# Kernel tuning notes

Measured on AMD Instinct MI355X. Metric: run time of the kernel, lower is better.

Reference implementation:

```python
import jax, jax.numpy as jnp
import numpy as np

BN_EPS = 1e-5

def _bn_train(h, gamma, beta):
    # h: [B, V, P, C]; BatchNorm2d in training mode: stats over (B, V, P) per channel
    mean = jnp.mean(h, axis=(0, 1, 2), keepdims=True)
    var = jnp.var(h, axis=(0, 1, 2), keepdims=True)
    return (h - mean) * jax.lax.rsqrt(var + BN_EPS) * gamma + beta

def _vfe(h, keep, W, b, gamma, beta):
    # h: [B,V,P,Cin] -> [B,V,P,2*units]; keep: [B,V,P,1] (1 = valid point)
    h = jnp.einsum('bvpc,cu->bvpu', h, W) + b
    h = jax.nn.relu(_bn_train(h, gamma, beta))
    agg = jnp.max(h, axis=2, keepdims=True)                 # [B,V,1,units]
    out = jnp.concatenate([h, jnp.broadcast_to(agg, h.shape)], axis=-1)
    return out * keep

def setup_inputs() -> dict:
    key = jax.random.key(0)
    ks = jax.random.split(key, 16)
    B, V, P, C = 1, 20000, 35, 7
    D, H, W = 10, 200, 176
    x = jax.random.normal(ks[0], (B, V, P, C), dtype=jnp.float32)
    cz = jax.random.randint(ks[1], (B, V, 1), 0, D)
    cy = jax.random.randint(ks[2], (B, V, 1), 0, H)
    cx = jax.random.randint(ks[3], (B, V, 1), 0, W)
    coordinate = jnp.concatenate([cz, cy, cx], axis=-1).astype(jnp.int32)
    def kaiming(k, fan_in, shape):
        bound = np.sqrt(6.0 / fan_in)
        return jax.random.uniform(k, shape, jnp.float32, -bound, bound)
    return {
        'x': x, 'coordinate': coordinate,
        'W1': kaiming(ks[4], 7, (7, 16)), 'b1': jnp.zeros((16,), jnp.float32),
        'g1': jnp.ones((16,), jnp.float32), 'be1': jnp.zeros((16,), jnp.float32),
        'W2': kaiming(ks[5], 32, (32, 64)), 'b2': jnp.zeros((64,), jnp.float32),
        'g2': jnp.ones((64,), jnp.float32), 'be2': jnp.zeros((64,), jnp.float32),
        'Wd': kaiming(ks[6], 128, (128, 128)), 'bd': jnp.zeros((128,), jnp.float32),
        'gd': jnp.ones((128,), jnp.float32), 'bed': jnp.zeros((128,), jnp.float32),
    }

def reference(x, coordinate, W1, b1, g1, be1, W2, b2, g2, be2, Wd, bd, gd, bed):
    D, H, W = 10, 200, 176
    # mask == 1 where point is empty (all-zero features)
    empty = (jnp.sum(x, axis=-1) == 0.0)[..., None].astype(jnp.float32)
    keep = 1.0 - empty
    h = _vfe(x, keep, W1, b1, g1, be1)    # [B,V,P,32]
    h = _vfe(h, keep, W2, b2, g2, be2)    # [B,V,P,128]
    h = jnp.einsum('bvpc,cu->bvpu', h, Wd) + bd
    h = jax.nn.relu(_bn_train(h, gd, bed))
    h = jnp.max(h, axis=2)                # [B,V,128] (max over points)
    feats = jnp.transpose(h, (0, 2, 1))   # [B,128,V]
    def scatter_one(coords, f):
        # f: [128,V]; coords: [V,3]; scatter-add into [128,D,H,W]
        g = jnp.zeros((128, D, H, W), dtype=f.dtype)
        return g.at[:, coords[:, 0], coords[:, 1], coords[:, 2]].add(f)
    grid = jax.vmap(scatter_one)(coordinate, feats)  # [B,128,D,H,W]
    return grid
```

## Files before the change

### kernel.cpp

```cpp
#include <hip/hip_runtime.h>
#include <float.h>

#define NV   20000
#define NP   35
#define NPTS 700000

#define S1SUM 0
#define S1SQ  16
#define S2SUM 32
#define S2SQ  96
#define S3SUM 160
#define S3SQ  288
#define SC1   416
#define SH1   432
#define SC2   448
#define SH2   512
#define SC3   576
#define SH3   704
#define M3MAX 1024
#define M3MIN (1024 + NV*128)

__global__ __launch_bounds__(256) void k_stats1(const float* __restrict__ x,
    const float* __restrict__ W1, const float* __restrict__ b1, float* __restrict__ ws)
{
  __shared__ float sW1[112], sb1[16];
  __shared__ float red[4][32];
  int t = threadIdx.x;
  if (t < 112) sW1[t] = W1[t];
  if (t < 16)  sb1[t] = b1[t];
  __syncthreads();
  float s[16], ss[16];
  #pragma unroll
  for (int u=0;u<16;++u){ s[u]=0.f; ss[u]=0.f; }
  int stride = gridDim.x * blockDim.x;
  for (int p = blockIdx.x*blockDim.x + t; p < NPTS; p += stride) {
    float xv[7];
    #pragma unroll
    for (int c=0;c<7;++c) xv[c] = x[p*7+c];
    #pragma unroll
    for (int u=0;u<16;++u) {
      float h = sb1[u];
      #pragma unroll
      for (int c=0;c<7;++c) h = fmaf(xv[c], sW1[c*16+u], h);
      s[u] += h; ss[u] = fmaf(h,h,ss[u]);
    }
  }
  #pragma unroll
  for (int u=0;u<16;++u) {
    #pragma unroll
    for (int off=32; off>0; off>>=1) {
      s[u]  += __shfl_xor(s[u],  off);
      ss[u] += __shfl_xor(ss[u], off);
    }
  }
  int wid = t>>6, lane = t&63;
  if (lane == 0) {
    #pragma unroll
    for (int u=0;u<16;++u){ red[wid][u]=s[u]; red[wid][16+u]=ss[u]; }
  }
  __syncthreads();
  if (t < 32) {
    float a = red[0][t]+red[1][t]+red[2][t]+red[3][t];
    atomicAdd(&ws[S1SUM + t], a);
  }
}

__global__ void k_finalize(const float* __restrict__ sum, const float* __restrict__ sq,
    const float* __restrict__ g, const float* __restrict__ be,
    float* __restrict__ scale, float* __restrict__ shift, int C)
{
  int u = threadIdx.x;
  if (u < C) {
    const float invN = 1.f/(float)NPTS;
    float mean = sum[u]*invN;
    float var  = sq[u]*invN - mean*mean;
    float sc = g[u] * rsqrtf(var + 1e-5f);
    scale[u] = sc;
    shift[u] = fmaf(-mean, sc, be[u]);
  }
}

template<int STAGE>
__global__ __launch_bounds__(256) void k_pass(
    const float* __restrict__ x,
    const float* __restrict__ W1, const float* __restrict__ b1,
    const float* __restrict__ W2, const float* __restrict__ b2,
    const float* __restrict__ Wd, const float* __restrict__ bd,
    float* __restrict__ ws)
{
  constexpr int NW = 4;
  __shared__ float sW1[112], sb1v[16], ssc1[16], ssh1[16];
  __shared__ __align__(16) float h1n_lds[NW][NP][20];
  __shared__ float keep_lds[NW][NP + 1];
  __shared__ __align__(16) float h2n_lds[STAGE==3 ? NW : 1][STAGE==3 ? NP : 1][64];
  __shared__ __align__(16) float agg2_lds[STAGE==3 ? NW : 1][64];
  __shared__ __align__(16) float sWd[STAGE==3 ? 128*128 : 4];

  int t = threadIdx.x;
  if (t < 112) sW1[t] = W1[t];
  if (t < 16) { sb1v[t]=b1[t]; ssc1[t]=ws[SC1+t]; ssh1[t]=ws[SH1+t]; }
  if constexpr (STAGE==3) {
    for (int i = t*4; i < 128*128; i += 256*4)
      *reinterpret_cast<float4*>(&sWd[i]) = *reinterpret_cast<const float4*>(&Wd[i]);
  }
  __syncthreads();

  int lane = t & 63, w = t >> 6;
  float W2r[32];
  #pragma unroll
  for (int c=0;c<32;++c) W2r[c] = W2[c*64 + lane];
  float b2r = b2[lane];
  float sc2r=0.f, sh2r=0.f, bdr0=0.f, bdr1=0.f;
  if constexpr (STAGE==3) {
    sc2r = ws[SC2+lane]; sh2r = ws[SH2+lane];
    bdr0 = bd[lane]; bdr1 = bd[64+lane];
  }
  float s2=0.f, ss2=0.f;
  float s3a=0.f, ss3a=0.f, s3b=0.f, ss3b=0.f;
  float* m3x = ws + M3MAX;
  float* m3n = ws + M3MIN;

  int wave = (blockIdx.x * blockDim.x + t) >> 6;
  int nw = (gridDim.x * blockDim.x) >> 6;
  for (int v = wave; v < NV; v += nw) {
    int p = lane;
    float xv[7];
    float kp = 0.f;
    if (p < NP) {
      float sum = 0.f;
      #pragma unroll
      for (int c=0;c<7;++c){ xv[c] = x[(v*NP + p)*7 + c]; sum += xv[c]; }
      kp = (sum == 0.f) ? 0.f : 1.f;
    } else {
      #pragma unroll
      for (int c=0;c<7;++c) xv[c]=0.f;
    }
    float h1v[16];
    #pragma unroll
    for (int u=0;u<16;++u) h1v[u] = sb1v[u];
    #pragma unroll
    for (int c=0;c<7;++c){
      float xc = xv[c];
      #pragma unroll
      for (int u=0;u<16;++u) h1v[u] = fmaf(xc, sW1[c*16+u], h1v[u]);
    }
    float aggv[16];
    #pragma unroll
    for (int u=0;u<16;++u){
      float hn = fmaxf(0.f, fmaf(h1v[u], ssc1[u], ssh1[u]));
      h1v[u] = hn;
      aggv[u] = (p < NP) ? hn : -FLT_MAX;
    }
    #pragma unroll
    for (int u=0;u<16;++u){
      #pragma unroll
      for (int off=32; off>0; off>>=1)
        aggv[u] = fmaxf(aggv[u], __shfl_xor(aggv[u], off));
    }
    if (p < NP) {
      #pragma unroll
      for (int c=0;c<16;c+=4)
        *reinterpret_cast<float4*>(&h1n_lds[w][p][c]) =
            make_float4(h1v[c],h1v[c+1],h1v[c+2],h1v[c+3]);
      keep_lds[w][p] = kp;
    }
    float t1 = 0.f;
    #pragma unroll
    for (int c=0;c<16;++c) t1 = fmaf(aggv[c], W2r[16+c], t1);
    float agg2u = -FLT_MAX;
    #pragma unroll
    for (int p2=0;p2<NP;++p2){
      float kpp = keep_lds[w][p2];
      float d = t1;
      #pragma unroll
      for (int c=0;c<16;c+=4){
        float4 a = *reinterpret_cast<const float4*>(&h1n_lds[w][p2][c]);
        d = fmaf(a.x, W2r[c],   d);
        d = fmaf(a.y, W2r[c+1], d);
        d = fmaf(a.z, W2r[c+2], d);
        d = fmaf(a.w, W2r[c+3], d);
      }
      float h2p = fmaf(kpp, d, b2r);
      if constexpr (STAGE==2) {
        s2 += h2p; ss2 = fmaf(h2p, h2p, ss2);
      } else {
        float h2nv = fmaxf(0.f, fmaf(h2p, sc2r, sh2r));
        agg2u = fmaxf(agg2u, h2nv);
        h2n_lds[w][p2][lane] = h2nv;
      }
    }
    if constexpr (STAGE==3) {
      agg2_lds[w][lane] = agg2u;
      float t3a=0.f, t3b=0.f;
      #pragma unroll
      for (int c=0;c<64;++c){
        float a = agg2_lds[w][c];
        t3a = fmaf(a, sWd[(64+c)*128 + lane],      t3a);
        t3b = fmaf(a, sWd[(64+c)*128 + 64 + lane], t3b);
      }
      float acc0[NP], acc1[NP];
      #pragma unroll
      for (int p2=0;p2<NP;++p2){ acc0[p2]=0.f; acc1[p2]=0.f; }
      for (int cb=0; cb<64; cb+=4){
        float w00=sWd[(cb+0)*128+lane],    w01=sWd[(cb+1)*128+lane],
              w02=sWd[(cb+2)*128+lane],    w03=sWd[(cb+3)*128+lane];
        float w10=sWd[(cb+0)*128+64+lane], w11=sWd[(cb+1)*128+64+lane],
              w12=sWd[(cb+2)*128+64+lane], w13=sWd[(cb+3)*128+64+lane];
        #pragma unroll
        for (int p2=0;p2<NP;++p2){
          float4 a = *reinterpret_cast<const float4*>(&h2n_lds[w][p2][cb]);
          acc0[p2] = fmaf(a.x,w00, fmaf(a.y,w01, fmaf(a.z,w02, fmaf(a.w,w03, acc0[p2]))));
          acc1[p2] = fmaf(a.x,w10, fmaf(a.y,w11, fmaf(a.z,w12, fmaf(a.w,w13, acc1[p2]))));
        }
      }
      float mx0=-FLT_MAX, mx1=-FLT_MAX, mn0=FLT_MAX, mn1=FLT_MAX;
      #pragma unroll
      for (int p2=0;p2<NP;++p2){
        float kpp = keep_lds[w][p2];
        float h0 = fmaf(kpp, acc0[p2]+t3a, bdr0);
        float h1 = fmaf(kpp, acc1[p2]+t3b, bdr1);
        s3a += h0; ss3a = fmaf(h0,h0,ss3a);
        s3b += h1; ss3b = fmaf(h1,h1,ss3b);
        mx0=fmaxf(mx0,h0); mn0=fminf(mn0,h0);
        mx1=fmaxf(mx1,h1); mn1=fminf(mn1,h1);
      }
      m3x[v*128+lane]    = mx0;  m3x[v*128+64+lane] = mx1;
      m3n[v*128+lane]    = mn0;  m3n[v*128+64+lane] = mn1;
    }
  }
  if constexpr (STAGE==2) {
    atomicAdd(&ws[S2SUM+lane], s2);
    atomicAdd(&ws[S2SQ +lane], ss2);
  } else {
    atomicAdd(&ws[S3SUM+lane],    s3a);
    atomicAdd(&ws[S3SUM+64+lane], s3b);
    atomicAdd(&ws[S3SQ+lane],     ss3a);
    atomicAdd(&ws[S3SQ+64+lane],  ss3b);
  }
}

__global__ __launch_bounds__(256) void k_scatter(const float* __restrict__ ws,
    const int* __restrict__ coord, float* __restrict__ out)
{
  int tid = blockIdx.x*blockDim.x + threadIdx.x;
  if (tid >= NV*128) return;
  int v = tid >> 7, u = tid & 127;
  float sc = ws[SC3+u], sh = ws[SH3+u];
  float m = (sc >= 0.f) ? ws[M3MAX+tid] : ws[M3MIN+tid];
  float val = fmaxf(0.f, fmaf(m, sc, sh));
  if (val != 0.f) {
    int z = coord[v*3+0], y = coord[v*3+1], xx = coord[v*3+2];
    atomicAdd(&out[((u*10+z)*200+y)*176+xx], val);
  }
}

extern "C" void kernel_launch(void* const* d_in, const int* in_sizes, int n_in,
                              void* d_out, int out_size, void* d_ws, size_t ws_size,
                              hipStream_t stream)
{
  const float* x   = (const float*)d_in[0];
  const int*   coord = (const int*)d_in[1];
  const float* W1  = (const float*)d_in[2];
  const float* b1  = (const float*)d_in[3];
  const float* g1  = (const float*)d_in[4];
  const float* be1 = (const float*)d_in[5];
  const float* W2  = (const float*)d_in[6];
  const float* b2  = (const float*)d_in[7];
  const float* g2  = (const float*)d_in[8];
  const float* be2 = (const float*)d_in[9];
  const float* Wd  = (const float*)d_in[10];
  const float* bd  = (const float*)d_in[11];
  const float* gd  = (const float*)d_in[12];
  const float* bed = (const float*)d_in[13];
  float* out = (float*)d_out;
  float* ws  = (float*)d_ws;

  hipMemsetAsync(ws, 0, 416*sizeof(float), stream);
  hipMemsetAsync(out, 0, (size_t)out_size*sizeof(float), stream);

  k_stats1<<<640,256,0,stream>>>(x, W1, b1, ws);
  k_finalize<<<1,128,0,stream>>>(ws+S1SUM, ws+S1SQ, g1, be1, ws+SC1, ws+SH1, 16);
  k_pass<2><<<1024,256,0,stream>>>(x, W1,b1,W2,b2,Wd,bd, ws);
  k_finalize<<<1,128,0,stream>>>(ws+S2SUM, ws+S2SQ, g2, be2, ws+SC2, ws+SH2, 64);
  k_pass<3><<<512,256,0,stream>>>(x, W1,b1,W2,b2,Wd,bd, ws);
  k_finalize<<<1,128,0,stream>>>(ws+S3SUM, ws+S3SQ, gd, bed, ws+SC3, ws+SH3, 128);
  k_scatter<<<(NV*128+255)/256,256,0,stream>>>(ws, coord, out);
}
```

Measured before the change: 986.8 us.

## Compute layer-1 BN stats from input moments and fold finalize kernels into consumers

Replaces the layer-1 stats kernel with one that accumulates the first and second moments of the 7 input channels (35 values). Each consumer block then derives the layer-1 mean and variance analytically from W1. The three tiny finalize launches are removed and their scale/shift computation is done redundantly at the start of the consuming kernels. Stage 3 moves to 512-thread blocks (8 waves) with half the grid, and the h1 LDS padding is shrunk from 20 to 16. This cuts launches and per-point matmul work in the stats pass, but E[x^2]-based variance may lose float precision, and the larger stage-3 blocks change occupancy and LDS use.

```diff
diff --git a/kernel.cpp b/kernel.cpp
--- a/kernel.cpp
+++ b/kernel.cpp
@@ -5,102 +5,103 @@
 #define NP   35
 #define NPTS 700000
 
-#define S1SUM 0
-#define S1SQ  16
 #define S2SUM 32
 #define S2SQ  96
 #define S3SUM 160
 #define S3SQ  288
-#define SC1   416
-#define SH1   432
-#define SC2   448
-#define SH2   512
-#define SC3   576
-#define SH3   704
+#define MOM   864
 #define M3MAX 1024
 #define M3MIN (1024 + NV*128)
 
-__global__ __launch_bounds__(256) void k_stats1(const float* __restrict__ x,
-    const float* __restrict__ W1, const float* __restrict__ b1, float* __restrict__ ws)
-{
-  __shared__ float sW1[112], sb1[16];
-  __shared__ float red[4][32];
+__global__ __launch_bounds__(256) void k_moments(const float* __restrict__ x,
+                                                 float* __restrict__ ws)
+{
+  float m[35];
+  #pragma unroll
+  for (int i=0;i<35;++i) m[i]=0.f;
+  int stride = gridDim.x*blockDim.x;
+  for (int p = blockIdx.x*blockDim.x + threadIdx.x; p < NPTS; p += stride) {
+    float xv[7];
+    #pragma unroll
+    for (int c=0;c<7;++c) xv[c]=x[p*7+c];
+    #pragma unroll
+    for (int c=0;c<7;++c) m[c] += xv[c];
+    int k=7;
+    #pragma unroll
+    for (int c=0;c<7;++c)
+      #pragma unroll
+      for (int d=c; d<7; ++d){ m[k]=fmaf(xv[c],xv[d],m[k]); ++k; }
+  }
+  #pragma unroll
+  for (int i=0;i<35;++i){
+    #pragma unroll
+    for (int off=32;off>0;off>>=1) m[i]+=__shfl_xor(m[i],off);
+  }
+  __shared__ float red[4][35];
+  int t=threadIdx.x, wv=t>>6, ln=t&63;
+  if (ln==0){
+    #pragma unroll
+    for (int i=0;i<35;++i) red[wv][i]=m[i];
+  }
+  __syncthreads();
+  if (t<35) atomicAdd(&ws[MOM+t], red[0][t]+red[1][t]+red[2][t]+red[3][t]);
+}
+
+template<int STAGE>
+__global__ __launch_bounds__(STAGE==3?512:256) void k_pass(
+    const float* __restrict__ x,
+    const float* __restrict__ W1, const float* __restrict__ b1,
+    const float* __restrict__ g1, const float* __restrict__ be1,
+    const float* __restrict__ W2, const float* __restrict__ b2,
+    const float* __restrict__ g2, const float* __restrict__ be2,
+    const float* __restrict__ Wd, const float* __restrict__ bd,
+    float* __restrict__ ws)
+{
+  constexpr int NW = (STAGE==3) ? 8 : 4;
+  constexpr int NT = NW*64;
+  __shared__ float sW1[112], sb1v[16], ssc1[16], ssh1[16];
+  __shared__ float ssc2[STAGE==3?64:1], ssh2[STAGE==3?64:1];
+  __shared__ __align__(16) float h1n_lds[NW][NP][16];
+  __shared__ float keep_lds[NW][NP+1];
+  __shared__ __align__(16) float h2n_lds[STAGE==3?NW:1][STAGE==3?NP:1][64];
+  __shared__ float agg2_lds[STAGE==3?NW:1][64];
+  __shared__ __align__(16) float sWd[STAGE==3?128*128:4];
+
   int t = threadIdx.x;
   if (t < 112) sW1[t] = W1[t];
-  if (t < 16)  sb1[t] = b1[t];
-  __syncthreads();
-  float s[16], ss[16];
-  #pragma unroll
-  for (int u=0;u<16;++u){ s[u]=0.f; ss[u]=0.f; }
-  int stride = gridDim.x * blockDim.x;
-  for (int p = blockIdx.x*blockDim.x + t; p < NPTS; p += stride) {
-    float xv[7];
-    #pragma unroll
-    for (int c=0;c<7;++c) xv[c] = x[p*7+c];
-    #pragma unroll
-    for (int u=0;u<16;++u) {
-      float h = sb1[u];
-      #pragma unroll
-      for (int c=0;c<7;++c) h = fmaf(xv[c], sW1[c*16+u], h);
-      s[u] += h; ss[u] = fmaf(h,h,ss[u]);
-    }
-  }
-  #pragma unroll
-  for (int u=0;u<16;++u) {
-    #pragma unroll
-    for (int off=32; off>0; off>>=1) {
-      s[u]  += __shfl_xor(s[u],  off);
-      ss[u] += __shfl_xor(ss[u], off);
-    }
-  }
-  int wid = t>>6, lane = t&63;
-  if (lane == 0) {
-    #pragma unroll
-    for (int u=0;u<16;++u){ red[wid][u]=s[u]; red[wid][16+u]=ss[u]; }
-  }
-  __syncthreads();
-  if (t < 32) {
-    float a = red[0][t]+red[1][t]+red[2][t]+red[3][t];
-    atomicAdd(&ws[S1SUM + t], a);
-  }
-}
-
-__global__ void k_finalize(const float* __restrict__ sum, const float* __restrict__ sq,
-    const float* __restrict__ g, const float* __restrict__ be,
-    float* __restrict__ scale, float* __restrict__ shift, int C)
-{
-  int u = threadIdx.x;
-  if (u < C) {
+  if (t < 16) {
+    sb1v[t] = b1[t];
     const float invN = 1.f/(float)NPTS;
-    float mean = sum[u]*invN;
-    float var  = sq[u]*invN - mean*mean;
-    float sc = g[u] * rsqrtf(var + 1e-5f);
-    scale[u] = sc;
-    shift[u] = fmaf(-mean, sc, be[u]);
-  }
-}
-
-template<int STAGE>
-__global__ __launch_bounds__(256) void k_pass(
-    const float* __restrict__ x,
-    const float* __restrict__ W1, const float* __restrict__ b1,
-    const float* __restrict__ W2, const float* __restrict__ b2,
-    const float* __restrict__ Wd, const float* __restrict__ bd,
-    float* __restrict__ ws)
-{
-  constexpr int NW = 4;
-  __shared__ float sW1[112], sb1v[16], ssc1[16], ssh1[16];
-  __shared__ __align__(16) float h1n_lds[NW][NP][20];
-  __shared__ float keep_lds[NW][NP + 1];
-  __shared__ __align__(16) float h2n_lds[STAGE==3 ? NW : 1][STAGE==3 ? NP : 1][64];
-  __shared__ __align__(16) float agg2_lds[STAGE==3 ? NW : 1][64];
-  __shared__ __align__(16) float sWd[STAGE==3 ? 128*128 : 4];
-
-  int t = threadIdx.x;
-  if (t < 112) sW1[t] = W1[t];
-  if (t < 16) { sb1v[t]=b1[t]; ssc1[t]=ws[SC1+t]; ssh1[t]=ws[SH1+t]; }
+    float wl[7], xb[7];
+    #pragma unroll
+    for (int c=0;c<7;++c){ wl[c]=W1[c*16+t]; xb[c]=ws[MOM+c]*invN; }
+    float ms=0.f;
+    #pragma unroll
+    for (int c=0;c<7;++c) ms = fmaf(wl[c], xb[c], ms);
+    const int base[7] = {0,7,13,18,22,25,27};
+    float e2=0.f;
+    #pragma unroll
+    for (int c=0;c<7;++c)
+      #pragma unroll
+      for (int d=0;d<7;++d){
+        int lo = c<d?c:d, hi = c<d?d:c;
+        e2 = fmaf(wl[c]*wl[d], ws[MOM+7+base[lo]+(hi-lo)]*invN, e2);
+      }
+    float var = e2 - ms*ms;
+    float sc = g1[t] * rsqrtf(var + 1e-5f);
+    ssc1[t] = sc;
+    ssh1[t] = fmaf(-(ms + b1[t]), sc, be1[t]);
+  }
   if constexpr (STAGE==3) {
-    for (int i = t*4; i < 128*128; i += 256*4)
+    if (t < 64) {
+      const float invN = 1.f/(float)NPTS;
+      float mean = ws[S2SUM+t]*invN;
+      float var  = ws[S2SQ+t]*invN - mean*mean;
+      float sc = g2[t]*rsqrtf(var+1e-5f);
+      ssc2[t] = sc;
+      ssh2[t] = fmaf(-mean, sc, be2[t]);
+    }
+    for (int i = t*4; i < 128*128; i += NT*4)
       *reinterpret_cast<float4*>(&sWd[i]) = *reinterpret_cast<const float4*>(&Wd[i]);
   }
   __syncthreads();
@@ -112,7 +113,7 @@
   float b2r = b2[lane];
   float sc2r=0.f, sh2r=0.f, bdr0=0.f, bdr1=0.f;
   if constexpr (STAGE==3) {
-    sc2r = ws[SC2+lane]; sh2r = ws[SH2+lane];
+    sc2r = ssc2[lane]; sh2r = ssh2[lane];
     bdr0 = bd[lane]; bdr1 = bd[64+lane];
   }
   float s2=0.f, ss2=0.f;
@@ -120,8 +121,8 @@
   float* m3x = ws + M3MAX;
   float* m3n = ws + M3MIN;
 
-  int wave = (blockIdx.x * blockDim.x + t) >> 6;
-  int nw = (gridDim.x * blockDim.x) >> 6;
+  int wave = (blockIdx.x * NT + t) >> 6;
+  int nw = (gridDim.x * NT) >> 6;
   for (int v = wave; v < NV; v += nw) {
     int p = lane;
     float xv[7];
@@ -240,12 +241,23 @@
 }
 
 __global__ __launch_bounds__(256) void k_scatter(const float* __restrict__ ws,
-    const int* __restrict__ coord, float* __restrict__ out)
-{
-  int tid = blockIdx.x*blockDim.x + threadIdx.x;
+    const int* __restrict__ coord, const float* __restrict__ gd,
+    const float* __restrict__ bed, float* __restrict__ out)
+{
+  __shared__ float s3c[128], s3h[128];
+  int t = threadIdx.x;
+  if (t < 128) {
+    const float invN = 1.f/(float)NPTS;
+    float mean = ws[S3SUM+t]*invN;
+    float var  = ws[S3SQ+t]*invN - mean*mean;
+    float sc = gd[t]*rsqrtf(var+1e-5f);
+    s3c[t]=sc; s3h[t]=fmaf(-mean,sc,bed[t]);
+  }
+  __syncthreads();
+  int tid = blockIdx.x*256 + t;
   if (tid >= NV*128) return;
   int v = tid >> 7, u = tid & 127;
-  float sc = ws[SC3+u], sh = ws[SH3+u];
+  float sc = s3c[u], sh = s3h[u];
   float m = (sc >= 0.f) ? ws[M3MAX+tid] : ws[M3MIN+tid];
   float val = fmaxf(0.f, fmaf(m, sc, sh));
   if (val != 0.f) {
@@ -275,14 +287,11 @@
   float* out = (float*)d_out;
   float* ws  = (float*)d_ws;
 
-  hipMemsetAsync(ws, 0, 416*sizeof(float), stream);
+  hipMemsetAsync(ws, 0, 1024*sizeof(float), stream);
   hipMemsetAsync(out, 0, (size_t)out_size*sizeof(float), stream);
 
-  k_stats1<<<640,256,0,stream>>>(x, W1, b1, ws);
-  k_finalize<<<1,128,0,stream>>>(ws+S1SUM, ws+S1SQ, g1, be1, ws+SC1, ws+SH1, 16);
-  k_pass<2><<<1024,256,0,stream>>>(x, W1,b1,W2,b2,Wd,bd, ws);
-  k_finalize<<<1,128,0,stream>>>(ws+S2SUM, ws+S2SQ, g2, be2, ws+SC2, ws+SH2, 64);
-  k_pass<3><<<512,256,0,stream>>>(x, W1,b1,W2,b2,Wd,bd, ws);
-  k_finalize<<<1,128,0,stream>>>(ws+S3SUM, ws+S3SQ, gd, bed, ws+SC3, ws+SH3, 128);
-  k_scatter<<<(NV*128+255)/256,256,0,stream>>>(ws, coord, out);
-}
+  k_moments<<<640,256,0,stream>>>(x, ws);
+  k_pass<2><<<1024,256,0,stream>>>(x, W1,b1,g1,be1, W2,b2,g2,be2, Wd,bd, ws);
+  k_pass<3><<<256,512,0,stream>>>(x, W1,b1,g1,be1, W2,b2,g2,be2, Wd,bd, ws);
+  k_scatter<<<10000,256,0,stream>>>(ws, coord, gd, bed, out);
+}
```

New measurement: 1.099 ms. 11.4% more time.
